# Optimization experiments

Hardware: AMD Instinct MI355X
Metric: run time of the kernel (lower is better)

The kernel has to match this reference:

```python
import jax, jax.numpy as jnp
import numpy as np

WS = 8          # window size
DIM = 192
NH = 6          # num heads
HD = DIM // NH  # head dim = 32
HIDDEN = 768    # mlp_ratio 4
EPS = 1e-5


def _rel_tables(ws):
    # continuous relative-coords table, shape (1, 2w-1, 2w-1, 2)
    r = np.arange(-(ws - 1), ws, dtype=np.float32)
    table = np.stack(np.meshgrid(r, r, indexing='ij'), axis=-1)[None]
    table = table / (ws - 1) * 8.0
    # relative position index, shape (N, N)
    coords = np.stack(np.meshgrid(np.arange(ws), np.arange(ws), indexing='ij'))
    cf = coords.reshape(2, -1)
    rel = (cf[:, :, None] - cf[:, None, :]).transpose(1, 2, 0).astype(np.int64)
    rel[:, :, 0] += ws - 1
    rel[:, :, 1] += ws - 1
    rel[:, :, 0] *= 2 * ws - 1
    idx = rel.sum(-1)
    return jnp.asarray(table), jnp.asarray(idx)

_TABLE, _RPI = _rel_tables(WS)


def _layernorm(x, g, b):
    m = jnp.mean(x, -1, keepdims=True)
    v = jnp.var(x, -1, keepdims=True)
    return (x - m) * jax.lax.rsqrt(v + EPS) * g + b


def setup_inputs() -> dict:
    key = jax.random.key(0)
    ks = jax.random.split(key, 12)
    B, H, W = 2, 256, 256
    s = 0.02
    return {
        'x': jax.random.normal(ks[0], (B, H * W, DIM), jnp.float32),
        'scale': jax.random.uniform(ks[1], (1, 2), jnp.float32, 0.5, 2.0),
        'norm1_g': jnp.ones((DIM,), jnp.float32),
        'norm1_b': jnp.zeros((DIM,), jnp.float32),
        'qkv_w': jax.random.normal(ks[2], (DIM, 3 * DIM), jnp.float32) * s,
        'qkv_b': jnp.zeros((3 * DIM,), jnp.float32),
        'proj_w': jax.random.normal(ks[3], (DIM, DIM), jnp.float32) * s,
        'proj_b': jnp.zeros((DIM,), jnp.float32),
        'cpb_w1': jax.random.normal(ks[4], (4, 512), jnp.float32) * s,
        'cpb_b1': jnp.zeros((512,), jnp.float32),
        'cpb_w2': jax.random.normal(ks[5], (512, NH), jnp.float32) * s,
        'cpb_b2': jnp.zeros((NH,), jnp.float32),
        'norm2_g': jnp.ones((DIM,), jnp.float32),
        'norm2_b': jnp.zeros((DIM,), jnp.float32),
        'fc1_w': jax.random.normal(ks[6], (DIM, HIDDEN), jnp.float32) * s,
        'fc1_b': jnp.zeros((HIDDEN,), jnp.float32),
        'fc2_w': jax.random.normal(ks[7], (HIDDEN, DIM), jnp.float32) * s,
        'fc2_b': jnp.zeros((DIM,), jnp.float32),
        'dw_w': jax.random.normal(ks[8], (HIDDEN, 1, 3, 3), jnp.float32) * s,
        'dw_b': jnp.zeros((HIDDEN,), jnp.float32),
        'H': 256,
        'W': 256,
    }


def reference(x, scale, norm1_g, norm1_b, qkv_w, qkv_b, proj_w, proj_b,
              cpb_w1, cpb_b1, cpb_w2, cpb_b2, norm2_g, norm2_b,
              fc1_w, fc1_b, fc2_w, fc2_b, dw_w, dw_b, H, W):
    B, L, C = x.shape
    N = WS * WS
    shortcut = x

    # ---- W-MSA branch ----
    h = _layernorm(x, norm1_g, norm1_b).reshape(B, H, W, C)
    # window partition -> (B*nW, N, C)
    h = h.reshape(B, H // WS, WS, W // WS, WS, C).transpose(0, 1, 3, 2, 4, 5)
    xw = h.reshape(-1, N, C)
    B_ = xw.shape[0]

    qkv = (xw @ qkv_w + qkv_b).reshape(B_, N, 3, NH, HD).transpose(2, 0, 3, 1, 4)
    q, k, v = qkv[0], qkv[1], qkv[2]          # (B_, NH, N, HD)
    q = q * (HD ** -0.5)
    attn = jnp.einsum('bhnd,bhmd->bhnm', q, k)  # (B_, NH, N, N)

    # continuous relative position bias from cpb MLP conditioned on `scale`
    rel_cell = jnp.broadcast_to(scale[:, None, None, :], _TABLE.shape)  # (1,2w-1,2w-1,2)
    coords4 = jnp.concatenate([_TABLE, rel_cell], axis=-1)              # (1,2w-1,2w-1,4)
    bias_tab = (jax.nn.relu(coords4 @ cpb_w1 + cpb_b1) @ cpb_w2 + cpb_b2).reshape(-1, NH)
    rpb = bias_tab[_RPI.reshape(-1)].reshape(N, N, NH).transpose(2, 0, 1)  # (NH,N,N)
    attn = jax.nn.softmax(attn + rpb[None], axis=-1)

    out = jnp.einsum('bhnm,bhmd->bhnd', attn, v).transpose(0, 2, 1, 3).reshape(B_, N, C)
    out = out @ proj_w + proj_b

    # window reverse
    out = out.reshape(B, H // WS, W // WS, WS, WS, C).transpose(0, 1, 3, 2, 4, 5)
    out = out.reshape(B, L, C)
    x = shortcut + out

    # ---- conv-augmented MLP branch ----
    h = _layernorm(x, norm2_g, norm2_b)
    h = jax.nn.gelu(h @ fc1_w + fc1_b, approximate=False)   # (B, L, HIDDEN)
    hc = h.transpose(0, 2, 1).reshape(B, HIDDEN, H, W)
    hc = jax.lax.conv_general_dilated(
        hc, dw_w, window_strides=(1, 1), padding=((1, 1), (1, 1)),
        dimension_numbers=('NCHW', 'OIHW', 'NCHW'), feature_group_count=HIDDEN)
    hc = hc + dw_b[None, :, None, None]
    h = hc.reshape(B, HIDDEN, L).transpose(0, 2, 1)
    h = jax.nn.gelu(h, approximate=False)
    h = h @ fc2_w + fc2_b
    return x + h
```

## Files before the change

kernel.cpp:

```cpp
#include <hip/hip_runtime.h>
#include <hip/hip_bf16.h>

typedef __attribute__((ext_vector_type(8))) short  bf16x8;
typedef __attribute__((ext_vector_type(4))) float  f32x4;
typedef __attribute__((ext_vector_type(8))) unsigned short u16x8;
typedef __attribute__((ext_vector_type(4))) unsigned short u16x4;

__device__ __forceinline__ unsigned short f2b(float f) {
    unsigned int u = __builtin_bit_cast(unsigned int, f);
    u += 0x7FFFu + ((u >> 16) & 1u);
    return (unsigned short)(u >> 16);
}
__device__ __forceinline__ float b2f(unsigned short u) {
    return __builtin_bit_cast(float, (unsigned int)u << 16);
}
__device__ __forceinline__ float gelu_fast(float x) {
    float d = 1.0f + __expf(-1.702f * x);
    return x * __builtin_amdgcn_rcpf(d);
}
__device__ __forceinline__ int wperm(int m) {
    int w = m >> 6, n = m & 63;
    int b = w >> 10, wy = (w >> 5) & 31, wx = w & 31;
    int y = wy * 8 + (n >> 3), xx = wx * 8 + (n & 7);
    return (b << 16) + (y << 8) + xx;
}

__device__ __forceinline__ void gload_lds16(const void* g, void* l) {
    __builtin_amdgcn_global_load_lds(
        (const __attribute__((address_space(1))) void*)g,
        (__attribute__((address_space(3))) void*)l, 16, 0, 0);
}

__global__ void transpose_w(const float* __restrict__ in, unsigned short* __restrict__ out,
                            int K, int N) {
    int i = blockIdx.x * 256 + threadIdx.x;
    if (i >= K * N) return;
    int n = i / K, k = i - n * K;
    out[i] = f2b(in[k * N + n]);
}

__global__ void transpose_wf(const float* __restrict__ in, float* __restrict__ out,
                             int K, int N) {
    int i = blockIdx.x * 256 + threadIdx.x;
    if (i >= K * N) return;
    int n = i / K, k = i - n * K;
    out[i] = in[k * N + n];
}

__global__ __launch_bounds__(256) void cpb_kernel(
    const float* __restrict__ scale, const float* __restrict__ w1, const float* __restrict__ b1,
    const float* __restrict__ w2, const float* __restrict__ b2, float* __restrict__ btab) {
    int t = threadIdx.x;
    if (t >= 225) return;
    int i = t / 15, j = t - (t / 15) * 15;
    float ti = (i - 7) * (8.0f / 7.0f);
    float tj = (j - 7) * (8.0f / 7.0f);
    float s0 = scale[0], s1 = scale[1];
    float acc[6];
    #pragma unroll
    for (int h = 0; h < 6; ++h) acc[h] = b2[h];
    for (int k = 0; k < 512; ++k) {
        float hv = ti * w1[k] + tj * w1[512 + k] + s0 * w1[1024 + k] + s1 * w1[1536 + k] + b1[k];
        hv = fmaxf(hv, 0.f);
        #pragma unroll
        for (int h = 0; h < 6; ++h) acc[h] += hv * w2[k * 6 + h];
    }
    #pragma unroll
    for (int h = 0; h < 6; ++h) btab[t * 6 + h] = acc[h];
}

template<int MODE>
__global__ __launch_bounds__(512) void gemm64(
    const float* __restrict__ Af, const unsigned short* __restrict__ Ab,
    const float* __restrict__ stats, const float* __restrict__ lng, const float* __restrict__ lnb,
    const unsigned short* __restrict__ Bt, const float* __restrict__ bias,
    unsigned short* __restrict__ oq, unsigned short* __restrict__ ok2, unsigned short* __restrict__ ov,
    const float* __restrict__ resid, float* __restrict__ ofp, unsigned short* __restrict__ obf,
    float* __restrict__ ostat) {
    constexpr int NCT = (MODE == 0) ? 3 : (MODE == 2) ? 4 : 1;
    __shared__ __align__(16) unsigned short Asw[3 * 64 * 64];
    __shared__ __align__(16) unsigned short Bsw[2 * 192 * 64];
    const int t = threadIdx.x, lane = t & 63, wv8 = t >> 6;
    const int wm = wv8 >> 2, wn = wv8 & 3;
    const int l15 = lane & 15, lq = lane >> 4;
    const int m0 = blockIdx.x * 64;

    int boffs[3];
    #pragma unroll
    for (int s = 0; s < 3; ++s) {
        int row = (wv8 + 8 * s) * 8 + (lane >> 3);
        boffs[s] = row * 192 + ((lane & 7) ^ (lane >> 3)) * 8;
    }
    if constexpr (MODE == 1) {
        #pragma unroll
        for (int s = 0; s < 3; ++s) {
            int si = wv8 + 8 * s;
            int row = (si & 7) * 8 + (lane >> 3);
            int src = (m0 + row) * 192 + (si >> 3) * 64 + ((lane & 7) ^ (lane >> 3)) * 8;
            gload_lds16(Ab + src, (char*)Asw + si * 1024);
        }
    }
    #pragma unroll
    for (int s = 0; s < 3; ++s)
        gload_lds16(Bt + boffs[s], (char*)Bsw + (wv8 + 8 * s) * 1024);

    if constexpr (MODE == 0) {
        int row = t >> 3, oct = t & 7;
        const float* p = Af + (size_t)wperm(m0 + row) * 192 + oct * 24;
        f32x4 v[6];
        float s = 0.f, q = 0.f;
        #pragma unroll
        for (int i = 0; i < 6; ++i) {
            v[i] = *(const f32x4*)(p + i * 4);
            #pragma unroll
            for (int j = 0; j < 4; ++j) { s += v[i][j]; q += v[i][j] * v[i][j]; }
        }
        s += __shfl_xor(s, 1); s += __shfl_xor(s, 2); s += __shfl_xor(s, 4);
        q += __shfl_xor(q, 1); q += __shfl_xor(q, 2); q += __shfl_xor(q, 4);
        float mean = s * (1.f / 192.f);
        float rstd = rsqrtf(q * (1.f / 192.f) - mean * mean + 1e-5f);
        #pragma unroll
        for (int i = 0; i < 6; ++i) {
            int k = oct * 24 + i * 4;
            u16x4 pk;
            #pragma unroll
            for (int j = 0; j < 4; ++j)
                pk[j] = f2b((v[i][j] - mean) * rstd * lng[k + j] + lnb[k + j]);
            int cc = k >> 6, ch = (k >> 2) & 15;
            int byte = cc * 8192 + row * 128 +
                       ((((ch >> 1) ^ (row & 7)) << 4) + ((ch & 1) << 3));
            *(u16x4*)((char*)Asw + byte) = pk;
        }
        asm volatile("s_waitcnt lgkmcnt(0)" ::: "memory");
    }

    const int axor = (l15 & 7) << 4;
    int cur = 0, it = 0;
    for (int ct = 0; ct < NCT; ++ct) {
        f32x4 acc[2][3];
        #pragma unroll
        for (int i = 0; i < 2; ++i)
            #pragma unroll
            for (int j = 0; j < 3; ++j) acc[i][j] = (f32x4){0.f, 0.f, 0.f, 0.f};
        for (int c = 0; c < 3; ++c, ++it) {
            if (it < NCT * 3 - 1) {
                int ctn = (c == 2) ? ct + 1 : ct;
                int cn  = (c == 2) ? 0 : c + 1;
                #pragma unroll
                for (int s = 0; s < 3; ++s)
                    gload_lds16(Bt + (size_t)ctn * 36864 + boffs[s] + cn * 64,
                                (char*)Bsw + (cur ^ 1) * 24576 + (wv8 + 8 * s) * 1024);
                asm volatile("s_waitcnt vmcnt(3)" ::: "memory");
            } else {
                asm volatile("s_waitcnt vmcnt(0)" ::: "memory");
            }
            __builtin_amdgcn_sched_barrier(0);
            __builtin_amdgcn_s_barrier();
            __builtin_amdgcn_sched_barrier(0);
            const char* Al = (const char*)Asw + c * 8192;
            const char* Bl = (const char*)Bsw + cur * 24576;
            #pragma unroll
            for (int kk = 0; kk < 2; ++kk) {
                bf16x8 a[2], bb[3];
                #pragma unroll
                for (int mt = 0; mt < 2; ++mt)
                    a[mt] = *(const bf16x8*)(Al + (wm * 32 + mt * 16 + l15) * 128 +
                                             ((kk << 6) ^ (lq << 4) ^ axor));
                #pragma unroll
                for (int nt = 0; nt < 3; ++nt)
                    bb[nt] = *(const bf16x8*)(Bl + (wn * 48 + nt * 16 + l15) * 128 +
                                              ((kk << 6) ^ (lq << 4) ^ axor));
                #pragma unroll
                for (int mt = 0; mt < 2; ++mt)
                    #pragma unroll
                    for (int nt = 0; nt < 3; ++nt)
                        acc[mt][nt] = __builtin_amdgcn_mfma_f32_16x16x32_bf16(a[mt], bb[nt], acc[mt][nt], 0, 0, 0);
            }
            __builtin_amdgcn_sched_barrier(0);
            __builtin_amdgcn_s_barrier();
            cur ^= 1;
        }
        if constexpr (MODE == 0) {
            unsigned short* dst = (ct == 0) ? oq : (ct == 1) ? ok2 : ov;
            float qs = (ct == 0) ? 0.17677669529663689f : 1.0f;
            #pragma unroll
            for (int mt = 0; mt < 2; ++mt)
                #pragma unroll
                for (int nt = 0; nt < 3; ++nt)
                    #pragma unroll
                    for (int r = 0; r < 4; ++r) {
                        int m = m0 + wm * 32 + mt * 16 + lq * 4 + r;
                        int col = wn * 48 + nt * 16 + l15;
                        float v = (acc[mt][nt][r] + bias[ct * 192 + col]) * qs;
                        int head = col >> 5, d = col & 31;
                        int w = m >> 6, n = m & 63;
                        dst[((size_t)(w * 6 + head) * 64 + n) * 32 + d] = f2b(v);
                    }
        }
    }
    (void)stats; (void)resid; (void)ofp; (void)obf; (void)ostat;
}

__global__ __launch_bounds__(512) void gemm_fused12(
    const unsigned short* __restrict__ Ab, const float* __restrict__ resid,
    const unsigned short* __restrict__ projT, const float* __restrict__ projb,
    const unsigned short* __restrict__ fc1T, const float* __restrict__ fc1b,
    const float* __restrict__ n2g, const float* __restrict__ n2b,
    float* __restrict__ ofp, unsigned short* __restrict__ obf) {
    __shared__ __align__(16) unsigned short Asw[3 * 64 * 64];
    __shared__ __align__(16) unsigned short Bsw[2 * 192 * 64];
    __shared__ float sred[64 * 8];
    __shared__ float srow[64 * 2];
    const int t = threadIdx.x, lane = t & 63, wv8 = t >> 6;
    const int wm = wv8 >> 2, wn = wv8 & 3;
    const int l15 = lane & 15, lq = lane >> 4;
    const int m0 = blockIdx.x * 64;

    int boffs[3];
    #pragma unroll
    for (int s = 0; s < 3; ++s) {
        int row = (wv8 + 8 * s) * 8 + (lane >> 3);
        boffs[s] = row * 192 + ((lane & 7) ^ (lane >> 3)) * 8;
    }
    #pragma unroll
    for (int s = 0; s < 3; ++s) {
        int si = wv8 + 8 * s;
        int row = (si & 7) * 8 + (lane >> 3);
        int src = (m0 + row) * 192 + (si >> 3) * 64 + ((lane & 7) ^ (lane >> 3)) * 8;
        gload_lds16(Ab + src, (char*)Asw + si * 1024);
    }
    #pragma unroll
    for (int s = 0; s < 3; ++s)
        gload_lds16(projT + boffs[s], (char*)Bsw + (wv8 + 8 * s) * 1024);

    const int axor = (l15 & 7) << 4;
    int cur = 0;

    f32x4 acc[2][3];
    #pragma unroll
    for (int i = 0; i < 2; ++i)
        #pragma unroll
        for (int j = 0; j < 3; ++j) acc[i][j] = (f32x4){0.f, 0.f, 0.f, 0.f};
    for (int c = 0; c < 3; ++c) {
        if (c < 2) {
            #pragma unroll
            for (int s = 0; s < 3; ++s)
                gload_lds16(projT + boffs[s] + (c + 1) * 64,
                            (char*)Bsw + (cur ^ 1) * 24576 + (wv8 + 8 * s) * 1024);
        } else {
            #pragma unroll
            for (int s = 0; s < 3; ++s)
                gload_lds16(fc1T + boffs[s],
                            (char*)Bsw + (cur ^ 1) * 24576 + (wv8 + 8 * s) * 1024);
        }
        asm volatile("s_waitcnt vmcnt(3)" ::: "memory");
        __builtin_amdgcn_sched_barrier(0);
        __builtin_amdgcn_s_barrier();
        __builtin_amdgcn_sched_barrier(0);
        const char* Al = (const char*)Asw + c * 8192;
        const char* Bl = (const char*)Bsw + cur * 24576;
        #pragma unroll
        for (int kk = 0; kk < 2; ++kk) {
            bf16x8 a[2], bb[3];
            #pragma unroll
            for (int mt = 0; mt < 2; ++mt)
                a[mt] = *(const bf16x8*)(Al + (wm * 32 + mt * 16 + l15) * 128 +
                                         ((kk << 6) ^ (lq << 4) ^ axor));
            #pragma unroll
            for (int nt = 0; nt < 3; ++nt)
                bb[nt] = *(const bf16x8*)(Bl + (wn * 48 + nt * 16 + l15) * 128 +
                                          ((kk << 6) ^ (lq << 4) ^ axor));
            #pragma unroll
            for (int mt = 0; mt < 2; ++mt)
                #pragma unroll
                for (int nt = 0; nt < 3; ++nt)
                    acc[mt][nt] = __builtin_amdgcn_mfma_f32_16x16x32_bf16(a[mt], bb[nt], acc[mt][nt], 0, 0, 0);
        }
        __builtin_amdgcn_sched_barrier(0);
        __builtin_amdgcn_s_barrier();
        cur ^= 1;
    }
    float w[2][3][4];
    #pragma unroll
    for (int mt = 0; mt < 2; ++mt) {
        #pragma unroll
        for (int r = 0; r < 4; ++r) {
            int row = wm * 32 + mt * 16 + lq * 4 + r;
            int r2 = wperm(m0 + row);
            float s = 0.f, q = 0.f;
            #pragma unroll
            for (int nt = 0; nt < 3; ++nt) {
                int col = wn * 48 + nt * 16 + l15;
                size_t idx = (size_t)r2 * 192 + col;
                float wv = resid[idx] + acc[mt][nt][r] + projb[col];
                ofp[idx] = wv;
                w[mt][nt][r] = wv;
                s += wv;
                q += wv * wv;
            }
            #pragma unroll
            for (int off = 1; off < 16; off <<= 1) {
                s += __shfl_xor(s, off);
                q += __shfl_xor(q, off);
            }
            if (l15 == 0) {
                sred[row * 8 + wn * 2]     = s;
                sred[row * 8 + wn * 2 + 1] = q;
            }
        }
    }
    __syncthreads();
    if (t < 64) {
        float s = sred[t * 8] + sred[t * 8 + 2] + sred[t * 8 + 4] + sred[t * 8 + 6];
        float q = sred[t * 8 + 1] + sred[t * 8 + 3] + sred[t * 8 + 5] + sred[t * 8 + 7];
        float mean = s * (1.f / 192.f);
        float var = q * (1.f / 192.f) - mean * mean;
        srow[t * 2] = mean;
        srow[t * 2 + 1] = rsqrtf(var + 1e-5f);
    }
    __syncthreads();
    {
        float g3[3], b3[3];
        #pragma unroll
        for (int nt = 0; nt < 3; ++nt) {
            int col = wn * 48 + nt * 16 + l15;
            g3[nt] = n2g[col];
            b3[nt] = n2b[col];
        }
        #pragma unroll
        for (int mt = 0; mt < 2; ++mt)
            #pragma unroll
            for (int r = 0; r < 4; ++r) {
                int row = wm * 32 + mt * 16 + lq * 4 + r;
                float mean = srow[row * 2], rstd = srow[row * 2 + 1];
                #pragma unroll
                for (int nt = 0; nt < 3; ++nt) {
                    int k = wn * 48 + nt * 16 + l15;
                    float nv = (w[mt][nt][r] - mean) * rstd * g3[nt] + b3[nt];
                    int cc = k >> 6, kk = k & 63;
                    int byte = cc * 8192 + row * 128 +
                               ((((kk >> 3) ^ (row & 7)) << 4) + (kk & 7) * 2);
                    *(unsigned short*)((char*)Asw + byte) = f2b(nv);
                }
            }
    }
    __syncthreads();

    for (int ct = 0; ct < 4; ++ct) {
        f32x4 a2[2][3];
        #pragma unroll
        for (int i = 0; i < 2; ++i)
            #pragma unroll
            for (int j = 0; j < 3; ++j) a2[i][j] = (f32x4){0.f, 0.f, 0.f, 0.f};
        for (int c = 0; c < 3; ++c) {
            int it = ct * 3 + c;
            if (it < 11) {
                int ctn = (c == 2) ? ct + 1 : ct;
                int cn  = (c == 2) ? 0 : c + 1;
                #pragma unroll
                for (int s = 0; s < 3; ++s)
                    gload_lds16(fc1T + (size_t)ctn * 36864 + boffs[s] + cn * 64,
                                (char*)Bsw + (cur ^ 1) * 24576 + (wv8 + 8 * s) * 1024);
                asm volatile("s_waitcnt vmcnt(3)" ::: "memory");
            } else {
                asm volatile("s_waitcnt vmcnt(0)" ::: "memory");
            }
            __builtin_amdgcn_sched_barrier(0);
            __builtin_amdgcn_s_barrier();
            __builtin_amdgcn_sched_barrier(0);
            const char* Al = (const char*)Asw + c * 8192;
            const char* Bl = (const char*)Bsw + cur * 24576;
            #pragma unroll
            for (int kk = 0; kk < 2; ++kk) {
                bf16x8 a[2], bb[3];
                #pragma unroll
                for (int mt = 0; mt < 2; ++mt)
                    a[mt] = *(const bf16x8*)(Al + (wm * 32 + mt * 16 + l15) * 128 +
                                             ((kk << 6) ^ (lq << 4) ^ axor));
                #pragma unroll
                for (int nt = 0; nt < 3; ++nt)
                    bb[nt] = *(const bf16x8*)(Bl + (wn * 48 + nt * 16 + l15) * 128 +
                                              ((kk << 6) ^ (lq << 4) ^ axor));
                #pragma unroll
                for (int mt = 0; mt < 2; ++mt)
                    #pragma unroll
                    for (int nt = 0; nt < 3; ++nt)
                        a2[mt][nt] = __builtin_amdgcn_mfma_f32_16x16x32_bf16(a[mt], bb[nt], a2[mt][nt], 0, 0, 0);
            }
            __builtin_amdgcn_sched_barrier(0);
            __builtin_amdgcn_s_barrier();
            cur ^= 1;
        }
        #pragma unroll
        for (int mt = 0; mt < 2; ++mt)
            #pragma unroll
            for (int nt = 0; nt < 3; ++nt)
                #pragma unroll
                for (int r = 0; r < 4; ++r) {
                    int m = m0 + wm * 32 + mt * 16 + lq * 4 + r;
                    int col = wn * 48 + nt * 16 + l15;
                    obf[(size_t)wperm(m) * 768 + ct * 192 + col] =
                        f2b(gelu_fast(a2[mt][nt][r] + fc1b[ct * 192 + col]));
                }
    }
}

__global__ __launch_bounds__(64) void attn_win(
    const unsigned short* __restrict__ qb, const unsigned short* __restrict__ kb,
    const unsigned short* __restrict__ vb, const float* __restrict__ btab,
    unsigned short* __restrict__ ao) {
    __shared__ float sb[225];
    __shared__ __align__(16) unsigned short pl[64 * 72];
    __shared__ __align__(16) unsigned short vT[32 * 72];
    const int bid = blockIdx.x;
    const int w = bid / 6, h = bid - w * 6;
    const int lane = threadIdx.x;
    const int l15 = lane & 15, lq = lane >> 4;

    for (int i = lane; i < 225; i += 64) sb[i] = btab[i * 6 + h];

    const unsigned short* qp = qb + (size_t)bid * 2048;
    const unsigned short* kp = kb + (size_t)bid * 2048;
    const unsigned short* vp = vb + (size_t)bid * 2048;

    bf16x8 qf[4], kf[4];
    #pragma unroll
    for (int i = 0; i < 4; ++i) {
        qf[i] = *(const bf16x8*)(qp + (i * 16 + l15) * 32 + lq * 8);
        kf[i] = *(const bf16x8*)(kp + (i * 16 + l15) * 32 + lq * 8);
    }
    #pragma unroll
    for (int i = 0; i < 4; ++i) {
        int c = lane + i * 64;
        int mr = c >> 2, d0 = (c & 3) * 8;
        u16x8 v = *(const u16x8*)(vp + mr * 32 + d0);
        #pragma unroll
        for (int j = 0; j < 8; ++j) vT[(d0 + j) * 72 + mr] = v[j];
    }
    f32x4 s[4][4];
    #pragma unroll
    for (int mt = 0; mt < 4; ++mt)
        #pragma unroll
        for (int nt = 0; nt < 4; ++nt)
            s[mt][nt] = __builtin_amdgcn_mfma_f32_16x16x32_bf16(
                qf[mt], kf[nt], (f32x4){0.f, 0.f, 0.f, 0.f}, 0, 0, 0);
    __syncthreads();
    #pragma unroll
    for (int mt = 0; mt < 4; ++mt) {
        #pragma unroll
        for (int r = 0; r < 4; ++r) {
            int n = mt * 16 + lq * 4 + r;
            int ny = n >> 3, nx = n & 7;
            float sv[4];
            float mx = -1e30f;
            #pragma unroll
            for (int nt = 0; nt < 4; ++nt) {
                int m = nt * 16 + l15;
                int idx = (ny - (m >> 3) + 7) * 15 + (nx - (m & 7) + 7);
                float val = s[mt][nt][r] + sb[idx];
                sv[nt] = val;
                mx = fmaxf(mx, val);
            }
            #pragma unroll
            for (int off = 1; off < 16; off <<= 1) mx = fmaxf(mx, __shfl_xor(mx, off));
            float sum = 0.f;
            #pragma unroll
            for (int nt = 0; nt < 4; ++nt) { sv[nt] = __expf(sv[nt] - mx); sum += sv[nt]; }
            #pragma unroll
            for (int off = 1; off < 16; off <<= 1) sum += __shfl_xor(sum, off);
            float inv = 1.f / sum;
            #pragma unroll
            for (int nt = 0; nt < 4; ++nt)
                pl[n * 72 + nt * 16 + l15] = f2b(sv[nt] * inv);
        }
    }
    __syncthreads();
    f32x4 o[4][2];
    #pragma unroll
    for (int i = 0; i < 4; ++i)
        #pragma unroll
        for (int j = 0; j < 2; ++j) o[i][j] = (f32x4){0.f, 0.f, 0.f, 0.f};
    #pragma unroll
    for (int mt = 0; mt < 4; ++mt)
        #pragma unroll
        for (int kk = 0; kk < 2; ++kk) {
            bf16x8 a = *(bf16x8*)&pl[(mt * 16 + l15) * 72 + kk * 32 + lq * 8];
            #pragma unroll
            for (int dt = 0; dt < 2; ++dt) {
                bf16x8 b = *(bf16x8*)&vT[(dt * 16 + l15) * 72 + kk * 32 + lq * 8];
                o[mt][dt] = __builtin_amdgcn_mfma_f32_16x16x32_bf16(a, b, o[mt][dt], 0, 0, 0);
            }
        }
    #pragma unroll
    for (int mt = 0; mt < 4; ++mt)
        #pragma unroll
        for (int dt = 0; dt < 2; ++dt)
            #pragma unroll
            for (int r = 0; r < 4; ++r) {
                int n = mt * 16 + lq * 4 + r;
                int d = dt * 16 + l15;
                ao[((size_t)w * 64 + n) * 192 + h * 32 + d] = f2b(o[mt][dt][r]);
            }
}

__global__ __launch_bounds__(512) void conv_fc2_v14(
    const unsigned short* __restrict__ m1, const float* __restrict__ dwwTf,
    const float* __restrict__ dwb, const unsigned short* __restrict__ fc2T,
    const float* __restrict__ fc2b, float* __restrict__ out) {
    __shared__ __align__(16) unsigned short Xs[26 * 512];
    __shared__ __align__(16) unsigned short As[128 * 72];
    __shared__ __align__(16) unsigned short Bsw[192 * 64];
    const int t = threadIdx.x;
    const int g = ((blockIdx.x & 7) << 7) + (blockIdx.x >> 3);
    const int b = g >> 9, yt = (g >> 3) & 63, xq = g & 7;
    const int y0 = yt * 4, x0 = xq * 32;
    const int cg = t & 7, lx = t >> 3;
    const int xx = lx & 31, yy0 = lx >> 5;
    const size_t ibase = (size_t)b * 65536;

    const int lane = t & 63, wv8 = t >> 6;
    const int wm = wv8 >> 1, wn = wv8 & 1;
    const int l15 = lane & 15, lq = lane >> 4;

    int xoff[4];
    #pragma unroll
    for (int s = 0; s < 4; ++s) {
        int seg = wv8 + 8 * s;
        int e = seg * 512 + lane * 8;
        e = min(e, 13048);
        int row = e / 2176;
        int rem = e - row * 2176;
        int px = rem >> 6, ch = rem & 63;
        int gy = min(max(y0 - 1 + row, 0), 255);
        int gx = min(max(x0 - 1 + px, 0), 255);
        xoff[s] = ((b << 16) + (gy << 8) + gx) * 768 + ch;
    }
    int boff[3];
    #pragma unroll
    for (int s = 0; s < 3; ++s) {
        int row = (wv8 + 8 * s) * 8 + (lane >> 3);
        boff[s] = row * 768 + ((lane & 7) ^ (lane >> 3)) * 8;
    }

    f32x4 acc[2][6];
    #pragma unroll
    for (int i = 0; i < 2; ++i)
        #pragma unroll
        for (int j = 0; j < 6; ++j) acc[i][j] = (f32x4){0.f, 0.f, 0.f, 0.f};

    #pragma unroll
    for (int s = 0; s < 4; ++s)
        if (wv8 + 8 * s < 26)
            gload_lds16(m1 + xoff[s], (char*)Xs + (wv8 + 8 * s) * 1024);
    #pragma unroll
    for (int s = 0; s < 3; ++s)
        gload_lds16(fc2T + boff[s], (char*)Bsw + (wv8 + 8 * s) * 1024);

    const int xb = xx * 128 + cg * 16;
    const int gxp = x0 + xx;
    const bool xok0 = gxp >= 1;
    const bool xok2 = gxp <= 254;
    const int oy0 = y0 + yy0;
    const int o00 = (lq * 16) ^ ((l15 & 7) << 4);
    const int brow = (wn * 96 + l15) * 128;

    for (int k0 = 0; k0 < 768; k0 += 64) {
        const int c0 = k0 + cg * 8;
        asm volatile("s_waitcnt vmcnt(0)" ::: "memory");
        __syncthreads();
        float a0[8], a1[8];
        #pragma unroll
        for (int j = 0; j < 8; ++j) { a0[j] = 0.f; a1[j] = 0.f; }
        #pragma unroll
        for (int kx = 0; kx < 3; ++kx) {
            if (kx == 0 && !xok0) continue;
            if (kx == 2 && !xok2) continue;
            #pragma unroll
            for (int ky = 0; ky < 3; ++ky) {
                const float* wp = dwwTf + (ky * 3 + kx) * 768 + c0;
                f32x4 w0 = *(const f32x4*)wp;
                f32x4 w1 = *(const f32x4*)(wp + 4);
                if ((unsigned)(oy0 + ky - 1) < 256u) {
                    u16x8 in = *(const u16x8*)((const char*)Xs +
                        (yy0 + ky) * 4352 + xb + kx * 128);
                    #pragma unroll
                    for (int j = 0; j < 4; ++j) {
                        a0[j]     += b2f(in[j]) * w0[j];
                        a0[4 + j] += b2f(in[4 + j]) * w1[j];
                    }
                }
                if ((unsigned)(oy0 + ky + 1) < 256u) {
                    u16x8 in = *(const u16x8*)((const char*)Xs +
                        (yy0 + 2 + ky) * 4352 + xb + kx * 128);
                    #pragma unroll
                    for (int j = 0; j < 4; ++j) {
                        a1[j]     += b2f(in[j]) * w0[j];
                        a1[4 + j] += b2f(in[4 + j]) * w1[j];
                    }
                }
            }
        }
        {
            f32x4 b0 = *(const f32x4*)(dwb + c0);
            f32x4 b1 = *(const f32x4*)(dwb + c0 + 4);
            u16x8 o0, o1;
            #pragma unroll
            for (int j = 0; j < 4; ++j) {
                o0[j]     = f2b(gelu_fast(a0[j] + b0[j]));
                o0[4 + j] = f2b(gelu_fast(a0[4 + j] + b1[j]));
                o1[j]     = f2b(gelu_fast(a1[j] + b0[j]));
                o1[4 + j] = f2b(gelu_fast(a1[4 + j] + b1[j]));
            }
            *(u16x8*)&As[lx * 72 + cg * 8] = o0;
            *(u16x8*)&As[(lx + 64) * 72 + cg * 8] = o1;
        }
        __syncthreads();
        if (k0 < 704) {
            #pragma unroll
            for (int s = 0; s < 4; ++s)
                if (wv8 + 8 * s < 26)
                    gload_lds16(m1 + xoff[s] + k0 + 64,
                                (char*)Xs + (wv8 + 8 * s) * 1024);
        }
        #pragma unroll
        for (int kk = 0; kk < 2; ++kk) {
            bf16x8 af[2];
            #pragma unroll
            for (int mt = 0; mt < 2; ++mt)
                af[mt] = *(bf16x8*)&As[(wm * 32 + mt * 16 + l15) * 72 + kk * 32 + lq * 8];
            #pragma unroll
            for (int nt = 0; nt < 6; ++nt) {
                bf16x8 bb = *(const bf16x8*)((const char*)Bsw + brow + nt * 2048 + (o00 ^ (kk << 6)));
                #pragma unroll
                for (int mt = 0; mt < 2; ++mt)
                    acc[mt][nt] = __builtin_amdgcn_mfma_f32_16x16x32_bf16(af[mt], bb, acc[mt][nt], 0, 0, 0);
            }
        }
        __syncthreads();
        if (k0 < 704) {
            #pragma unroll
            for (int s = 0; s < 3; ++s)
                gload_lds16(fc2T + boff[s] + k0 + 64, (char*)Bsw + (wv8 + 8 * s) * 1024);
        }
    }
    #pragma unroll
    for (int mt = 0; mt < 2; ++mt)
        #pragma unroll
        for (int nt = 0; nt < 6; ++nt)
            #pragma unroll
            for (int r = 0; r < 4; ++r) {
                int ml = wm * 32 + mt * 16 + lq * 4 + r;
                int py = ml >> 5, lxx = ml & 31;
                int col = wn * 96 + nt * 16 + l15;
                size_t idx = (ibase + (size_t)(y0 + py) * 256 + x0 + lxx) * 192 + col;
                out[idx] = out[idx] + acc[mt][nt][r] + fc2b[col];
            }
}

extern "C" void kernel_launch(void* const* d_in, const int* in_sizes, int n_in,
                              void* d_out, int out_size, void* d_ws, size_t ws_size,
                              hipStream_t stream) {
    (void)in_sizes; (void)n_in; (void)out_size; (void)ws_size;
    const float* x     = (const float*)d_in[0];
    const float* scale = (const float*)d_in[1];
    const float* n1g   = (const float*)d_in[2];
    const float* n1b   = (const float*)d_in[3];
    const float* qkvw  = (const float*)d_in[4];
    const float* qkvb  = (const float*)d_in[5];
    const float* projw = (const float*)d_in[6];
    const float* projb = (const float*)d_in[7];
    const float* cw1   = (const float*)d_in[8];
    const float* cb1   = (const float*)d_in[9];
    const float* cw2   = (const float*)d_in[10];
    const float* cb2   = (const float*)d_in[11];
    const float* n2g   = (const float*)d_in[12];
    const float* n2b   = (const float*)d_in[13];
    const float* fc1w  = (const float*)d_in[14];
    const float* fc1b  = (const float*)d_in[15];
    const float* fc2w  = (const float*)d_in[16];
    const float* fc2b  = (const float*)d_in[17];
    const float* dww   = (const float*)d_in[18];
    const float* dwb   = (const float*)d_in[19];
    float* out = (float*)d_out;

    char* ws = (char*)d_ws;
    unsigned short* qkvT  = (unsigned short*)ws;
    unsigned short* projT = qkvT + 110592;
    unsigned short* fc1T  = projT + 36864;
    unsigned short* fc2T  = fc1T + 147456;
    float* btab   = (float*)(ws + 1048576);
    float* dwwTf  = (float*)(ws + 1310720);
    unsigned short* pool = (unsigned short*)(ws + 4194304);
    const size_t S = 25165824;
    unsigned short* qb = pool;
    unsigned short* kb = pool + S;
    unsigned short* vb = pool + 2 * S;
    unsigned short* ab = pool + 3 * S;
    unsigned short* m1 = pool;

    transpose_w<<<432, 256, 0, stream>>>(qkvw, qkvT, 192, 576);
    transpose_w<<<144, 256, 0, stream>>>(projw, projT, 192, 192);
    transpose_w<<<576, 256, 0, stream>>>(fc1w, fc1T, 192, 768);
    transpose_w<<<576, 256, 0, stream>>>(fc2w, fc2T, 768, 192);
    transpose_wf<<<27, 256, 0, stream>>>(dww, dwwTf, 768, 9);
    cpb_kernel<<<1, 256, 0, stream>>>(scale, cw1, cb1, cw2, cb2, btab);

    gemm64<0><<<2048, 512, 0, stream>>>(
        x, (const unsigned short*)nullptr, (const float*)nullptr, n1g, n1b,
        qkvT, qkvb,
        qb, kb, vb, (const float*)nullptr, (float*)nullptr, (unsigned short*)nullptr,
        (float*)nullptr);
    attn_win<<<12288, 64, 0, stream>>>(qb, kb, vb, btab, ab);
    gemm_fused12<<<2048, 512, 0, stream>>>(
        ab, x, projT, projb, fc1T, fc1b, n2g, n2b, out, m1);
    conv_fc2_v14<<<1024, 512, 0, stream>>>(m1, dwwTf, dwb, fc2T, fc2b, out);
}
```

Baseline: 564.5 us.

## Fuse window attention into proj+fc1 kernel, dropping attention output buffer

Window attention is folded into the proj/LN2/fc1 GEMM kernel. Each 512-thread block handles one window, with six waves computing one head each. The attention output is written straight into the swizzled LDS A-tile, so the separate attn_win launch and the global round trip of its bf16 output go away. In exchange, two of the eight waves sit idle during the attention phase, extra barriers are added, and m1 moves to a separate pool region. gemm64 also loses its unused modes and parameters.

```diff
diff --git a/kernel.cpp b/kernel.cpp
--- a/kernel.cpp
+++ b/kernel.cpp
@@ -71,13 +71,11 @@
 
 template<int MODE>
 __global__ __launch_bounds__(512) void gemm64(
-    const float* __restrict__ Af, const unsigned short* __restrict__ Ab,
-    const float* __restrict__ stats, const float* __restrict__ lng, const float* __restrict__ lnb,
+    const float* __restrict__ Af,
+    const float* __restrict__ lng, const float* __restrict__ lnb,
     const unsigned short* __restrict__ Bt, const float* __restrict__ bias,
-    unsigned short* __restrict__ oq, unsigned short* __restrict__ ok2, unsigned short* __restrict__ ov,
-    const float* __restrict__ resid, float* __restrict__ ofp, unsigned short* __restrict__ obf,
-    float* __restrict__ ostat) {
-    constexpr int NCT = (MODE == 0) ? 3 : (MODE == 2) ? 4 : 1;
+    unsigned short* __restrict__ oq, unsigned short* __restrict__ ok2, unsigned short* __restrict__ ov) {
+    constexpr int NCT = 3;
     __shared__ __align__(16) unsigned short Asw[3 * 64 * 64];
     __shared__ __align__(16) unsigned short Bsw[2 * 192 * 64];
     const int t = threadIdx.x, lane = t & 63, wv8 = t >> 6;
@@ -91,20 +89,11 @@
         int row = (wv8 + 8 * s) * 8 + (lane >> 3);
         boffs[s] = row * 192 + ((lane & 7) ^ (lane >> 3)) * 8;
     }
-    if constexpr (MODE == 1) {
-        #pragma unroll
-        for (int s = 0; s < 3; ++s) {
-            int si = wv8 + 8 * s;
-            int row = (si & 7) * 8 + (lane >> 3);
-            int src = (m0 + row) * 192 + (si >> 3) * 64 + ((lane & 7) ^ (lane >> 3)) * 8;
-            gload_lds16(Ab + src, (char*)Asw + si * 1024);
-        }
-    }
     #pragma unroll
     for (int s = 0; s < 3; ++s)
         gload_lds16(Bt + boffs[s], (char*)Bsw + (wv8 + 8 * s) * 1024);
 
-    if constexpr (MODE == 0) {
+    {
         int row = t >> 3, oct = t & 7;
         const float* p = Af + (size_t)wperm(m0 + row) * 192 + oct * 24;
         f32x4 v[6];
@@ -180,42 +169,146 @@
             __builtin_amdgcn_s_barrier();
             cur ^= 1;
         }
-        if constexpr (MODE == 0) {
-            unsigned short* dst = (ct == 0) ? oq : (ct == 1) ? ok2 : ov;
-            float qs = (ct == 0) ? 0.17677669529663689f : 1.0f;
-            #pragma unroll
-            for (int mt = 0; mt < 2; ++mt)
-                #pragma unroll
-                for (int nt = 0; nt < 3; ++nt)
-                    #pragma unroll
-                    for (int r = 0; r < 4; ++r) {
-                        int m = m0 + wm * 32 + mt * 16 + lq * 4 + r;
-                        int col = wn * 48 + nt * 16 + l15;
-                        float v = (acc[mt][nt][r] + bias[ct * 192 + col]) * qs;
-                        int head = col >> 5, d = col & 31;
-                        int w = m >> 6, n = m & 63;
-                        dst[((size_t)(w * 6 + head) * 64 + n) * 32 + d] = f2b(v);
-                    }
-        }
-    }
-    (void)stats; (void)resid; (void)ofp; (void)obf; (void)ostat;
-}
-
-__global__ __launch_bounds__(512) void gemm_fused12(
-    const unsigned short* __restrict__ Ab, const float* __restrict__ resid,
+        unsigned short* dst = (ct == 0) ? oq : (ct == 1) ? ok2 : ov;
+        float qs = (ct == 0) ? 0.17677669529663689f : 1.0f;
+        #pragma unroll
+        for (int mt = 0; mt < 2; ++mt)
+            #pragma unroll
+            for (int nt = 0; nt < 3; ++nt)
+                #pragma unroll
+                for (int r = 0; r < 4; ++r) {
+                    int m = m0 + wm * 32 + mt * 16 + lq * 4 + r;
+                    int col = wn * 48 + nt * 16 + l15;
+                    float v = (acc[mt][nt][r] + bias[ct * 192 + col]) * qs;
+                    int head = col >> 5, d = col & 31;
+                    int w = m >> 6, n = m & 63;
+                    dst[((size_t)(w * 6 + head) * 64 + n) * 32 + d] = f2b(v);
+                }
+    }
+}
+
+__global__ __launch_bounds__(512) void attn_proj_fc1(
+    const unsigned short* __restrict__ qb, const unsigned short* __restrict__ kb,
+    const unsigned short* __restrict__ vb, const float* __restrict__ btab,
+    const float* __restrict__ resid,
     const unsigned short* __restrict__ projT, const float* __restrict__ projb,
     const unsigned short* __restrict__ fc1T, const float* __restrict__ fc1b,
     const float* __restrict__ n2g, const float* __restrict__ n2b,
     float* __restrict__ ofp, unsigned short* __restrict__ obf) {
     __shared__ __align__(16) unsigned short Asw[3 * 64 * 64];
     __shared__ __align__(16) unsigned short Bsw[2 * 192 * 64];
-    __shared__ float sred[64 * 8];
-    __shared__ float srow[64 * 2];
+    __shared__ float scratch[1352];
     const int t = threadIdx.x, lane = t & 63, wv8 = t >> 6;
     const int wm = wv8 >> 2, wn = wv8 & 3;
     const int l15 = lane & 15, lq = lane >> 4;
-    const int m0 = blockIdx.x * 64;
-
+    const int win = blockIdx.x;
+    const int m0 = win * 64;
+    const int axor = (l15 & 7) << 4;
+
+    for (int i = t; i < 1350; i += 512) {
+        int h = i / 225, idx = i - h * 225;
+        scratch[i] = btab[idx * 6 + h];
+    }
+    __syncthreads();
+
+    f32x4 o[4][2];
+    if (wv8 < 6) {
+        const size_t bid = (size_t)(win * 6 + wv8);
+        const unsigned short* qp = qb + bid * 2048;
+        const unsigned short* kp = kb + bid * 2048;
+        const unsigned short* vp = vb + bid * 2048;
+        bf16x8 qf[4], kf[4];
+        #pragma unroll
+        for (int i = 0; i < 4; ++i) {
+            qf[i] = *(const bf16x8*)(qp + (i * 16 + l15) * 32 + lq * 8);
+            kf[i] = *(const bf16x8*)(kp + (i * 16 + l15) * 32 + lq * 8);
+        }
+        #pragma unroll
+        for (int i = 0; i < 4; ++i) {
+            int c = lane + i * 64;
+            int mr = c >> 2, d0 = (c & 3) * 8;
+            u16x8 v = *(const u16x8*)(vp + mr * 32 + d0);
+            #pragma unroll
+            for (int j = 0; j < 8; ++j) {
+                int row = d0 + j;
+                int byte = wv8 * 4096 + row * 128 +
+                           (((mr >> 3) ^ (row & 7)) << 4) + (mr & 7) * 2;
+                *(unsigned short*)((char*)Asw + byte) = v[j];
+            }
+        }
+        #pragma unroll
+        for (int mt = 0; mt < 4; ++mt) {
+            f32x4 s[4];
+            #pragma unroll
+            for (int nt = 0; nt < 4; ++nt)
+                s[nt] = __builtin_amdgcn_mfma_f32_16x16x32_bf16(
+                    qf[mt], kf[nt], (f32x4){0.f, 0.f, 0.f, 0.f}, 0, 0, 0);
+            #pragma unroll
+            for (int r = 0; r < 4; ++r) {
+                int n = mt * 16 + lq * 4 + r;
+                int ny = n >> 3, nx = n & 7;
+                float sv[4];
+                float mx = -1e30f;
+                #pragma unroll
+                for (int nt = 0; nt < 4; ++nt) {
+                    int m = nt * 16 + l15;
+                    int idx = (ny - (m >> 3) + 7) * 15 + (nx - (m & 7) + 7);
+                    float val = s[nt][r] + scratch[wv8 * 225 + idx];
+                    sv[nt] = val;
+                    mx = fmaxf(mx, val);
+                }
+                #pragma unroll
+                for (int off = 1; off < 16; off <<= 1) mx = fmaxf(mx, __shfl_xor(mx, off));
+                float sum = 0.f;
+                #pragma unroll
+                for (int nt = 0; nt < 4; ++nt) { sv[nt] = __expf(sv[nt] - mx); sum += sv[nt]; }
+                #pragma unroll
+                for (int off = 1; off < 16; off <<= 1) sum += __shfl_xor(sum, off);
+                float inv = 1.f / sum;
+                #pragma unroll
+                for (int nt = 0; nt < 4; ++nt) {
+                    int col = nt * 16 + l15;
+                    int byte = wv8 * 8192 + n * 128 +
+                               (((col >> 3) ^ (n & 7)) << 4) + (col & 7) * 2;
+                    *(unsigned short*)((char*)Bsw + byte) = f2b(sv[nt] * inv);
+                }
+            }
+        }
+        asm volatile("s_waitcnt lgkmcnt(0)" ::: "memory");
+        #pragma unroll
+        for (int i = 0; i < 4; ++i)
+            #pragma unroll
+            for (int j = 0; j < 2; ++j) o[i][j] = (f32x4){0.f, 0.f, 0.f, 0.f};
+        #pragma unroll
+        for (int mt = 0; mt < 4; ++mt)
+            #pragma unroll
+            for (int kk = 0; kk < 2; ++kk) {
+                bf16x8 a = *(const bf16x8*)((char*)Bsw + wv8 * 8192 +
+                    (mt * 16 + l15) * 128 + ((kk << 6) ^ (lq << 4) ^ axor));
+                #pragma unroll
+                for (int dt = 0; dt < 2; ++dt) {
+                    bf16x8 b = *(const bf16x8*)((char*)Asw + wv8 * 4096 +
+                        (dt * 16 + l15) * 128 + ((kk << 6) ^ (lq << 4) ^ axor));
+                    o[mt][dt] = __builtin_amdgcn_mfma_f32_16x16x32_bf16(a, b, o[mt][dt], 0, 0, 0);
+                }
+            }
+    }
+    __syncthreads();
+    if (wv8 < 6) {
+        #pragma unroll
+        for (int mt = 0; mt < 4; ++mt)
+            #pragma unroll
+            for (int dt = 0; dt < 2; ++dt)
+                #pragma unroll
+                for (int r = 0; r < 4; ++r) {
+                    int row = mt * 16 + lq * 4 + r;
+                    int k = wv8 * 32 + dt * 16 + l15;
+                    int cc = k >> 6, k6 = k & 63;
+                    int byte = cc * 8192 + row * 128 +
+                               (((k6 >> 3) ^ (row & 7)) << 4) + (k6 & 7) * 2;
+                    *(unsigned short*)((char*)Asw + byte) = f2b(o[mt][dt][r]);
+                }
+    }
     int boffs[3];
     #pragma unroll
     for (int s = 0; s < 3; ++s) {
@@ -223,19 +316,11 @@
         boffs[s] = row * 192 + ((lane & 7) ^ (lane >> 3)) * 8;
     }
     #pragma unroll
-    for (int s = 0; s < 3; ++s) {
-        int si = wv8 + 8 * s;
-        int row = (si & 7) * 8 + (lane >> 3);
-        int src = (m0 + row) * 192 + (si >> 3) * 64 + ((lane & 7) ^ (lane >> 3)) * 8;
-        gload_lds16(Ab + src, (char*)Asw + si * 1024);
-    }
-    #pragma unroll
     for (int s = 0; s < 3; ++s)
         gload_lds16(projT + boffs[s], (char*)Bsw + (wv8 + 8 * s) * 1024);
-
-    const int axor = (l15 & 7) << 4;
+    __syncthreads();
+
     int cur = 0;
-
     f32x4 acc[2][3];
     #pragma unroll
     for (int i = 0; i < 2; ++i)
@@ -280,7 +365,9 @@
         __builtin_amdgcn_s_barrier();
         cur ^= 1;
     }
-    float w[2][3][4];
+    float* sred = scratch;
+    float* srow = scratch + 512;
+    float hw[2][3][4];
     #pragma unroll
     for (int mt = 0; mt < 2; ++mt) {
         #pragma unroll
@@ -294,7 +381,7 @@
                 size_t idx = (size_t)r2 * 192 + col;
                 float wv = resid[idx] + acc[mt][nt][r] + projb[col];
                 ofp[idx] = wv;
-                w[mt][nt][r] = wv;
+                hw[mt][nt][r] = wv;
                 s += wv;
                 q += wv * wv;
             }
@@ -336,10 +423,10 @@
                 #pragma unroll
                 for (int nt = 0; nt < 3; ++nt) {
                     int k = wn * 48 + nt * 16 + l15;
-                    float nv = (w[mt][nt][r] - mean) * rstd * g3[nt] + b3[nt];
-                    int cc = k >> 6, kk = k & 63;
+                    float nv = (hw[mt][nt][r] - mean) * rstd * g3[nt] + b3[nt];
+                    int cc = k >> 6, k6 = k & 63;
                     int byte = cc * 8192 + row * 128 +
-                               ((((kk >> 3) ^ (row & 7)) << 4) + (kk & 7) * 2);
+                               (((k6 >> 3) ^ (row & 7)) << 4) + (k6 & 7) * 2;
                     *(unsigned short*)((char*)Asw + byte) = f2b(nv);
                 }
             }
@@ -403,104 +490,6 @@
                         f2b(gelu_fast(a2[mt][nt][r] + fc1b[ct * 192 + col]));
                 }
     }
-}
-
-__global__ __launch_bounds__(64) void attn_win(
-    const unsigned short* __restrict__ qb, const unsigned short* __restrict__ kb,
-    const unsigned short* __restrict__ vb, const float* __restrict__ btab,
-    unsigned short* __restrict__ ao) {
-    __shared__ float sb[225];
-    __shared__ __align__(16) unsigned short pl[64 * 72];
-    __shared__ __align__(16) unsigned short vT[32 * 72];
-    const int bid = blockIdx.x;
-    const int w = bid / 6, h = bid - w * 6;
-    const int lane = threadIdx.x;
-    const int l15 = lane & 15, lq = lane >> 4;
-
-    for (int i = lane; i < 225; i += 64) sb[i] = btab[i * 6 + h];
-
-    const unsigned short* qp = qb + (size_t)bid * 2048;
-    const unsigned short* kp = kb + (size_t)bid * 2048;
-    const unsigned short* vp = vb + (size_t)bid * 2048;
-
-    bf16x8 qf[4], kf[4];
-    #pragma unroll
-    for (int i = 0; i < 4; ++i) {
-        qf[i] = *(const bf16x8*)(qp + (i * 16 + l15) * 32 + lq * 8);
-        kf[i] = *(const bf16x8*)(kp + (i * 16 + l15) * 32 + lq * 8);
-    }
-    #pragma unroll
-    for (int i = 0; i < 4; ++i) {
-        int c = lane + i * 64;
-        int mr = c >> 2, d0 = (c & 3) * 8;
-        u16x8 v = *(const u16x8*)(vp + mr * 32 + d0);
-        #pragma unroll
-        for (int j = 0; j < 8; ++j) vT[(d0 + j) * 72 + mr] = v[j];
-    }
-    f32x4 s[4][4];
-    #pragma unroll
-    for (int mt = 0; mt < 4; ++mt)
-        #pragma unroll
-        for (int nt = 0; nt < 4; ++nt)
-            s[mt][nt] = __builtin_amdgcn_mfma_f32_16x16x32_bf16(
-                qf[mt], kf[nt], (f32x4){0.f, 0.f, 0.f, 0.f}, 0, 0, 0);
-    __syncthreads();
-    #pragma unroll
-    for (int mt = 0; mt < 4; ++mt) {
-        #pragma unroll
-        for (int r = 0; r < 4; ++r) {
-            int n = mt * 16 + lq * 4 + r;
-            int ny = n >> 3, nx = n & 7;
-            float sv[4];
-            float mx = -1e30f;
-            #pragma unroll
-            for (int nt = 0; nt < 4; ++nt) {
-                int m = nt * 16 + l15;
-                int idx = (ny - (m >> 3) + 7) * 15 + (nx - (m & 7) + 7);
-                float val = s[mt][nt][r] + sb[idx];
-                sv[nt] = val;
-                mx = fmaxf(mx, val);
-            }
-            #pragma unroll
-            for (int off = 1; off < 16; off <<= 1) mx = fmaxf(mx, __shfl_xor(mx, off));
-            float sum = 0.f;
-            #pragma unroll
-            for (int nt = 0; nt < 4; ++nt) { sv[nt] = __expf(sv[nt] - mx); sum += sv[nt]; }
-            #pragma unroll
-            for (int off = 1; off < 16; off <<= 1) sum += __shfl_xor(sum, off);
-            float inv = 1.f / sum;
-            #pragma unroll
-            for (int nt = 0; nt < 4; ++nt)
-                pl[n * 72 + nt * 16 + l15] = f2b(sv[nt] * inv);
-        }
-    }
-    __syncthreads();
-    f32x4 o[4][2];
-    #pragma unroll
-    for (int i = 0; i < 4; ++i)
-        #pragma unroll
-        for (int j = 0; j < 2; ++j) o[i][j] = (f32x4){0.f, 0.f, 0.f, 0.f};
-    #pragma unroll
-    for (int mt = 0; mt < 4; ++mt)
-        #pragma unroll
-        for (int kk = 0; kk < 2; ++kk) {
-            bf16x8 a = *(bf16x8*)&pl[(mt * 16 + l15) * 72 + kk * 32 + lq * 8];
-            #pragma unroll
-            for (int dt = 0; dt < 2; ++dt) {
-                bf16x8 b = *(bf16x8*)&vT[(dt * 16 + l15) * 72 + kk * 32 + lq * 8];
-                o[mt][dt] = __builtin_amdgcn_mfma_f32_16x16x32_bf16(a, b, o[mt][dt], 0, 0, 0);
-            }
-        }
-    #pragma unroll
-    for (int mt = 0; mt < 4; ++mt)
-        #pragma unroll
-        for (int dt = 0; dt < 2; ++dt)
-            #pragma unroll
-            for (int r = 0; r < 4; ++r) {
-                int n = mt * 16 + lq * 4 + r;
-                int d = dt * 16 + l15;
-                ao[((size_t)w * 64 + n) * 192 + h * 32 + d] = f2b(o[mt][dt][r]);
-            }
 }
 
 __global__ __launch_bounds__(512) void conv_fc2_v14(
@@ -695,8 +684,7 @@
     unsigned short* qb = pool;
     unsigned short* kb = pool + S;
     unsigned short* vb = pool + 2 * S;
-    unsigned short* ab = pool + 3 * S;
-    unsigned short* m1 = pool;
+    unsigned short* m1 = pool + 3 * S;
 
     transpose_w<<<432, 256, 0, stream>>>(qkvw, qkvT, 192, 576);
     transpose_w<<<144, 256, 0, stream>>>(projw, projT, 192, 192);
@@ -705,13 +693,8 @@
     transpose_wf<<<27, 256, 0, stream>>>(dww, dwwTf, 768, 9);
     cpb_kernel<<<1, 256, 0, stream>>>(scale, cw1, cb1, cw2, cb2, btab);
 
-    gemm64<0><<<2048, 512, 0, stream>>>(
-        x, (const unsigned short*)nullptr, (const float*)nullptr, n1g, n1b,
-        qkvT, qkvb,
-        qb, kb, vb, (const float*)nullptr, (float*)nullptr, (unsigned short*)nullptr,
-        (float*)nullptr);
-    attn_win<<<12288, 64, 0, stream>>>(qb, kb, vb, btab, ab);
-    gemm_fused12<<<2048, 512, 0, stream>>>(
-        ab, x, projT, projb, fc1T, fc1b, n2g, n2b, out, m1);
+    gemm64<0><<<2048, 512, 0, stream>>>(x, n1g, n1b, qkvT, qkvb, qb, kb, vb);
+    attn_proj_fc1<<<2048, 512, 0, stream>>>(
+        qb, kb, vb, btab, x, projT, projb, fc1T, fc1b, n2g, n2b, out, m1);
     conv_fc2_v14<<<1024, 512, 0, stream>>>(m1, dwwTf, dwb, fc2T, fc2b, out);
 }
```

After: 553.2 us. -2.0%, faster.
